# Optimization experiments

Measured on AMD Instinct MI355X. Metric: run time of the kernel, lower is better.

## Reference

```python
import jax, jax.numpy as jnp
import numpy as np

K = 3
STRIDE = 1
PAD = 1


def _conv2d(x, w, b):
    y = jax.lax.conv_general_dilated(
        x, w, window_strides=(STRIDE, STRIDE),
        padding=[(PAD, PAD), (PAD, PAD)],
        dimension_numbers=("NCHW", "OIHW", "NCHW"))
    return y + b[None, :, None, None]


def _bilinear_sample(xb, py, px):
    # xb: [C, H, W]; py, px: [K2, Ho, Wo] float sample coords
    C, H, W = xb.shape
    y0 = jnp.floor(py)
    x0 = jnp.floor(px)
    ay = py - y0  # frac weights
    ax = px - x0
    out = jnp.zeros((C,) + py.shape, dtype=xb.dtype)
    corners = [
        (y0, x0, (1.0 - ay) * (1.0 - ax)),
        (y0, x0 + 1.0, (1.0 - ay) * ax),
        (y0 + 1.0, x0, ay * (1.0 - ax)),
        (y0 + 1.0, x0 + 1.0, ay * ax),
    ]
    for yc, xc, wgt in corners:
        valid = (yc >= 0) & (yc < H) & (xc >= 0) & (xc < W)
        yi = jnp.clip(yc, 0, H - 1).astype(jnp.int32)
        xi = jnp.clip(xc, 0, W - 1).astype(jnp.int32)
        g = xb[:, yi, xi]  # [C, K2, Ho, Wo]
        out = out + g * (wgt * valid.astype(xb.dtype))[None]
    return out


def _deform_forward(x, weight, bias, p_weight, p_bias):
    B, Cin, H, W = x.shape
    Cout = weight.shape[0]
    K2 = K * K
    # offset / mask prediction conv
    pout = _conv2d(x, p_weight, p_bias)  # [B, 3*K2, Ho, Wo]
    o1, o2, m = jnp.split(pout, 3, axis=1)
    offset = jnp.concatenate([o1, o2], axis=1)  # [B, 2*K2, Ho, Wo]
    mask = jax.nn.sigmoid(m)  # [B, K2, Ho, Wo]
    Ho, Wo = mask.shape[2], mask.shape[3]
    # torchvision layout: channel 2k = dy_k, 2k+1 = dx_k
    off = offset.reshape(B, K2, 2, Ho, Wo)
    dy, dx = off[:, :, 0], off[:, :, 1]  # [B, K2, Ho, Wo]
    ki = (jnp.arange(K2) // K).astype(x.dtype)  # kernel row
    kj = (jnp.arange(K2) % K).astype(x.dtype)   # kernel col
    base_y = jnp.arange(Ho, dtype=x.dtype) * STRIDE - PAD  # [Ho]
    base_x = jnp.arange(Wo, dtype=x.dtype) * STRIDE - PAD  # [Wo]
    py = base_y[None, None, :, None] + ki[None, :, None, None] + dy
    px = base_x[None, None, None, :] + kj[None, :, None, None] + dx
    sampled = jax.vmap(_bilinear_sample)(x, py, px)  # [B, Cin, K2, Ho, Wo]
    sampled = sampled * mask[:, None]
    w = weight.reshape(Cout, Cin, K2)
    out = jnp.einsum('bckhw,ock->bohw', sampled, w) + bias[None, :, None, None]
    return out


def setup_inputs() -> dict:
    key = jax.random.key(0)
    k1, k2, k3 = jax.random.split(key, 3)
    B, Cin, Cout, H, W = 4, 256, 256, 64, 64
    x = jax.random.normal(k1, (B, Cin, H, W), dtype=jnp.float32)
    fan_in = Cin * K * K
    weight = jax.random.normal(k2, (Cout, Cin, K, K), dtype=jnp.float32) / np.sqrt(fan_in)
    bias = jnp.zeros((Cout,), dtype=jnp.float32)
    # small random offset/mask predictor (zero-init in the original; randomized
    # here so the deformable sampling path is exercised)
    p_weight = jax.random.normal(k3, (3 * K * K, Cin, K, K), dtype=jnp.float32) * 0.02
    p_bias = jnp.zeros((3 * K * K,), dtype=jnp.float32)
    return {"x": x, "weight": weight, "bias": bias, "p_weight": p_weight, "p_bias": p_bias}


def reference(x, weight, bias, p_weight, p_bias):
    return _deform_forward(x, weight, bias, p_weight, p_bias)
```

## Files before the change

kernel.cpp:

```cpp
#include <hip/hip_runtime.h>
#include <stdint.h>


#define CIN 256
#define COUT 256
#define HWS 4096
#define MTOT 16384
#define KTOT 2304
#define SPLITK 8

typedef __attribute__((ext_vector_type(8))) short bf16x8;
typedef __attribute__((ext_vector_type(4))) float f32x4;

__device__ __forceinline__ unsigned short f2bf(float f) {
  unsigned int u = __float_as_uint(f);
  unsigned int r = (u + 0x7fffu + ((u >> 16) & 1u)) >> 16;
  return (unsigned short)r;
}
__device__ __forceinline__ float bf2f(unsigned short u) {
  return __uint_as_float(((unsigned int)u) << 16);
}
__device__ __forceinline__ float bflo(unsigned int u) { return __uint_as_float(u << 16); }
__device__ __forceinline__ float bfhi(unsigned int u) { return __uint_as_float(u & 0xffff0000u); }

__device__ __forceinline__ void gload_lds16(const void* g, void* l) {
  __builtin_amdgcn_global_load_lds((const __attribute__((address_space(1))) void*)g,
                                   (__attribute__((address_space(3))) void*)l, 16, 0, 0);
}

#define GLOAD8(D, P)  asm volatile("global_load_dwordx2 %0, %1, off" : "=v"(D) : "v"(P))
#define GLOAD16(D, P) asm volatile("global_load_dwordx4 %0, %1, off" : "=v"(D) : "v"(P))
#define WAITVM(N)                                            \
  {                                                          \
    asm volatile("s_waitcnt vmcnt(" #N ")" ::: "memory");    \
    __builtin_amdgcn_sched_barrier(0);                       \
  }
#define BARRIER_LGKM                                                  \
  { asm volatile("s_waitcnt lgkmcnt(0)\n\ts_barrier" ::: "memory"); }

__global__ __launch_bounds__(256) void prep_and_transpose(const float* __restrict__ x,
                                                          const float* __restrict__ w,
                                                          const float* __restrict__ pw,
                                                          unsigned short* __restrict__ xt,
                                                          unsigned short* __restrict__ WB,
                                                          unsigned short* __restrict__ PWs,
                                                          unsigned short* __restrict__ zerop) {
  __shared__ float tile[32][33];
  int bid = blockIdx.x;
  if (bid < 4096) {
    int b = bid >> 10;
    int rest = bid & 1023;
    int hw0 = (rest & 127) * 32;
    int c0 = ((rest >> 7) & 7) * 32;
    int tx = threadIdx.x & 31, ty = threadIdx.x >> 5;
    for (int i = ty; i < 32; i += 8)
      tile[i][tx] = x[(size_t)(b * CIN + c0 + i) * HWS + hw0 + tx];
    __syncthreads();
    for (int r = ty; r < 32; r += 8)
      xt[(size_t)(b * HWS + hw0 + r) * CIN + c0 + tx] = f2bf(tile[tx][r]);
  } else {
    int idx = (bid - 4096) * 256 + threadIdx.x;
    if (idx < 512)
      *(uint4*)(zerop + idx * 8) = make_uint4(0, 0, 0, 0);
    if (idx < KTOT * COUT) {
      int f = idx;
      int e = f & 7;
      int row = (f >> 3) & 15;
      int quad = (f >> 7) & 3;
      int j = (f >> 9) & 15;
      int t = f >> 13;
      int kk = t * 32 + quad * 8 + e;
      int o = j * 16 + row;
      int k = kk >> 8, c = kk & 255;
      WB[f] = f2bf(w[o * KTOT + c * 9 + k]);
    } else {
      int f2 = idx - KTOT * COUT;
      int t_ = f2 & 7;
      int rest = f2 >> 3;
      int j = rest & 31;
      int kk = (rest >> 5) * 8 + t_;
      int k = kk >> 8, c = kk & 255;
      float v = (j < 27) ? pw[j * KTOT + c * 9 + k] : 0.0f;
      PWs[f2] = f2bf(v);
    }
  }
}

__global__ __launch_bounds__(256) void offset_conv_sk(const unsigned short* __restrict__ xt,
                                                      const unsigned short* __restrict__ PWs,
                                                      const unsigned short* __restrict__ zerop,
                                                      float* __restrict__ Pbuf) {
  __shared__ unsigned short Al[64 * 32];
  __shared__ unsigned short Bl[1024];
  int tid = threadIdx.x;
  int lane = tid & 63, wv = tid >> 6;
  int mt = (blockIdx.x & 7) * 32 + (blockIdx.x >> 3);
  int m0 = mt * 64;
  int s = blockIdx.y;
  int b = m0 >> 12;
  int hw0 = m0 & 4095;
  f32x4 acc[2] = {};

  for (int tt = 0; tt < 72 / SPLITK; ++tt) {
    int t = s * (72 / SPLITK) + tt;
    int k = t >> 3, c0 = (t & 7) * 32;
    int dyk = k / 3 - 1;
    int dxk = k % 3 - 1;
    __syncthreads();
    if (tid < 128)
      gload_lds16(PWs + (size_t)t * 1024 + tid * 8, &Bl[tid * 8]);
    {
      int r = tid >> 2;
      int hw = hw0 + r;
      int h = hw >> 6, wwp = hw & 63;
      int y = h + dyk, xx = wwp + dxk;
      bool valid = ((unsigned)y < 64u) && ((unsigned)xx < 64u);
      const unsigned short* src = valid
          ? xt + ((size_t)((b << 12) + (y << 6) + xx) << 8) + c0 + (tid & 3) * 8
          : zerop;
      gload_lds16(src, &Al[tid * 8]);
    }
    __syncthreads();
    int row = lane & 15, quad = lane >> 4;
    bf16x8 af = *(const bf16x8*)&Al[(wv * 16 + row) * 32 + quad * 8];
    for (int j = 0; j < 2; ++j) {
      bf16x8 bfr = *(const bf16x8*)&Bl[(quad * 32 + j * 16 + row) * 8];
      acc[j] = __builtin_amdgcn_mfma_f32_16x16x32_bf16(af, bfr, acc[j], 0, 0, 0);
    }
  }

  int row = lane & 15, quad = lane >> 4;
  for (int j = 0; j < 2; ++j) {
    int n = j * 16 + row;
    for (int r_ = 0; r_ < 4; ++r_) {
      int m = m0 + wv * 16 + quad * 4 + r_;
      Pbuf[((size_t)s * MTOT + m) * 32 + n] = acc[j][r_];
    }
  }
}

__global__ __launch_bounds__(256) void index_prep(const float* __restrict__ Pbuf,
                                                  const float* __restrict__ p_bias,
                                                  int4* __restrict__ DIW) {
  int gid = blockIdx.x * 256 + threadIdx.x;
  int m = gid / 9;
  int k = gid - m * 9;

  float dy = p_bias[2 * k];
  float dx = p_bias[2 * k + 1];
  float mv = p_bias[18 + k];
#pragma unroll
  for (int s = 0; s < SPLITK; ++s) {
    const float* p = Pbuf + ((size_t)s * MTOT + m) * 32;
    dy += p[2 * k];
    dx += p[2 * k + 1];
    mv += p[18 + k];
  }
  float mk = 1.0f / (1.0f + __expf(-mv));

  int hw = m & 4095, h = hw >> 6, ww = hw & 63;
  float py = (float)(h - 1 + k / 3) + dy;
  float px = (float)(ww - 1 + k % 3) + dx;
  float y0f = floorf(py), x0f = floorf(px);
  float ay = py - y0f, ax = px - x0f;
  int y0 = (int)y0f, x0 = (int)x0f;

  float w00 = (1.f - ay) * (1.f - ax) * mk;
  float w01 = (1.f - ay) * ax * mk;
  float w10 = ay * (1.f - ax) * mk;
  float w11 = ay * ax * mk;

  float vy0 = ((unsigned)y0 < 64u) ? 1.f : 0.f;
  float vy1 = ((unsigned)(y0 + 1) < 64u) ? 1.f : 0.f;
  float vx0 = ((unsigned)x0 < 64u) ? 1.f : 0.f;
  float vx1 = ((unsigned)(x0 + 1) < 64u) ? 1.f : 0.f;
  w00 *= vy0 * vx0; w01 *= vy0 * vx1; w10 *= vy1 * vx0; w11 *= vy1 * vx1;

  int yc0 = min(max(y0, 0), 63), yc1 = min(max(y0 + 1, 0), 63);
  int xc0 = min(max(x0, 0), 63), xc1 = min(max(x0 + 1, 0), 63);

  DIW[(size_t)gid * 2] = make_int4((yc0 * 64 + xc0) * 256, (yc0 * 64 + xc1) * 256,
                                   (yc1 * 64 + xc0) * 256, (yc1 * 64 + xc1) * 256);
  float4 w4 = make_float4(w00, w01, w10, w11);
  ((float4*)DIW)[(size_t)gid * 2 + 1] = w4;
}

__device__ __forceinline__ void bilin4p(const uint2 c00, const uint2 c01,
                                        const uint2 c10, const uint2 c11,
                                        const float4 w4, unsigned short* dst) {
  float v0 = w4.x * bflo(c00.x) + w4.y * bflo(c01.x) + w4.z * bflo(c10.x) + w4.w * bflo(c11.x);
  float v1 = w4.x * bfhi(c00.x) + w4.y * bfhi(c01.x) + w4.z * bfhi(c10.x) + w4.w * bfhi(c11.x);
  float v2 = w4.x * bflo(c00.y) + w4.y * bflo(c01.y) + w4.z * bflo(c10.y) + w4.w * bflo(c11.y);
  float v3 = w4.x * bfhi(c00.y) + w4.y * bfhi(c01.y) + w4.z * bfhi(c10.y) + w4.w * bfhi(c11.y);
  ushort4 o;
  o.x = f2bf(v0); o.y = f2bf(v1); o.z = f2bf(v2); o.w = f2bf(v3);
  *(ushort4*)dst = o;
}

#define MFMA8(A0, A1, A2_, A3, B0, B1)                                                   \
  acc[0][0] = __builtin_amdgcn_mfma_f32_16x16x32_bf16(A0, B0, acc[0][0], 0, 0, 0);       \
  acc[0][1] = __builtin_amdgcn_mfma_f32_16x16x32_bf16(A0, B1, acc[0][1], 0, 0, 0);       \
  acc[1][0] = __builtin_amdgcn_mfma_f32_16x16x32_bf16(A1, B0, acc[1][0], 0, 0, 0);       \
  acc[1][1] = __builtin_amdgcn_mfma_f32_16x16x32_bf16(A1, B1, acc[1][1], 0, 0, 0);       \
  acc[2][0] = __builtin_amdgcn_mfma_f32_16x16x32_bf16(A2_, B0, acc[2][0], 0, 0, 0);      \
  acc[2][1] = __builtin_amdgcn_mfma_f32_16x16x32_bf16(A2_, B1, acc[2][1], 0, 0, 0);      \
  acc[3][0] = __builtin_amdgcn_mfma_f32_16x16x32_bf16(A3, B0, acc[3][0], 0, 0, 0);       \
  acc[3][1] = __builtin_amdgcn_mfma_f32_16x16x32_bf16(A3, B1, acc[3][1], 0, 0, 0);

#define FITER_S(T, PAR, GI0, GI1, GI2, GI3, GC0, GC1, GC2, GC3, BC0, BC1, BN0, BN1)      \
  {                                                                                      \
    if ((((T) + 2) & 7) == 0) dI4 = Tbl[r][((T) + 2) >> 3][0];                           \
    int cq = (((T) + 2) & 7) * 32 + qo;                                                  \
    GLOAD8(GI0, xtb + dI4.x + cq);                                                       \
    GLOAD8(GI1, xtb + dI4.y + cq);                                                       \
    GLOAD8(GI2, xtb + dI4.z + cq);                                                       \
    GLOAD8(GI3, xtb + dI4.w + cq);                                                       \
    const unsigned short* bt_ = bpb + (size_t)((T) + 1) * 8192;                          \
    GLOAD16(BN0, bt_);                                                                   \
    GLOAD16(BN1, bt_ + 512);                                                             \
    afr0 = *(const bf16x8*)&As[PAR][row][quad * 8];                                      \
    afr1 = *(const bf16x8*)&As[PAR][16 + row][quad * 8];                                 \
    afr2 = *(const bf16x8*)&As[PAR][32 + row][quad * 8];                                 \
    afr3 = *(const bf16x8*)&As[PAR][48 + row][quad * 8];                                 \
    if ((((T) + 1) & 7) == 0) dW4 = *(float4*)&Tbl[r][((T) + 1) >> 3][1];                \
    WAITVM(8)                                                                            \
    bilin4p(GC0, GC1, GC2, GC3, dW4, &As[PAR ^ 1][r][qo]);                               \
    WAITVM(6)                                                                            \
    MFMA8(afr0, afr1, afr2, afr3, BC0, BC1)                                              \
    BARRIER_LGKM                                                                         \
  }

__global__ __launch_bounds__(512, 2) void fused_gemm(const unsigned short* __restrict__ xt,
                                                     const int4* __restrict__ DIW,
                                                     const unsigned short* __restrict__ WB,
                                                     const float* __restrict__ bias,
                                                     float* __restrict__ out) {
  __shared__ unsigned short As[2][64][40];
  __shared__ int4 Tbl[64][9][2];

  int tid = threadIdx.x;
  int lane = tid & 63, wv = tid >> 6;
  int mt = (blockIdx.x & 7) * 32 + (blockIdx.x >> 3);
  int mb = mt * 64;
  int b = mb >> 12;
  int hw0 = mb & 4095;
  const unsigned short* xtb = xt + ((size_t)b << 20);

  {
    const int4* src = DIW + (size_t)mb * 18;
    int4* dst = (int4*)Tbl;
    for (int i = tid; i < 1152; i += 512)
      gload_lds16(src + i, dst + i);
  }
  __syncthreads();

  int r = tid >> 3;
  int qo = (tid & 7) * 4;

  int4 dI4 = Tbl[r][0][0];
  float4 dW4 = *(float4*)&Tbl[r][0][1];

  int row = lane & 15, quad = lane >> 4;
  const unsigned short* bpb = WB + (size_t)(wv * 2) * 512 + quad * 128 + row * 8;

  f32x4 acc[4][2] = {};
  uint2 gA0, gA1, gA2, gA3;
  uint2 gB0, gB1, gB2, gB3;
  bf16x8 bA0, bA1, bB0, bB1;
  bf16x8 afr0, afr1, afr2, afr3;

  {
    uint2 p00 = *(const uint2*)(xtb + dI4.x + qo);
    uint2 p01 = *(const uint2*)(xtb + dI4.y + qo);
    uint2 p10 = *(const uint2*)(xtb + dI4.z + qo);
    uint2 p11 = *(const uint2*)(xtb + dI4.w + qo);
    bilin4p(p00, p01, p10, p11, dW4, &As[0][r][qo]);
    GLOAD8(gB0, xtb + dI4.x + 32 + qo);
    GLOAD8(gB1, xtb + dI4.y + 32 + qo);
    GLOAD8(gB2, xtb + dI4.z + 32 + qo);
    GLOAD8(gB3, xtb + dI4.w + 32 + qo);
    GLOAD16(bA0, bpb);
    GLOAD16(bA1, bpb + 512);
  }
  BARRIER_LGKM

#pragma unroll 1
  for (int t = 0; t < 70; t += 2) {
    FITER_S(t,     0, gA0, gA1, gA2, gA3, gB0, gB1, gB2, gB3, bA0, bA1, bB0, bB1)
    FITER_S(t + 1, 1, gB0, gB1, gB2, gB3, gA0, gA1, gA2, gA3, bB0, bB1, bA0, bA1)
  }

  {
    const unsigned short* bt_ = bpb + (size_t)71 * 8192;
    GLOAD16(bB0, bt_);
    GLOAD16(bB1, bt_ + 512);
    afr0 = *(const bf16x8*)&As[0][row][quad * 8];
    afr1 = *(const bf16x8*)&As[0][16 + row][quad * 8];
    afr2 = *(const bf16x8*)&As[0][32 + row][quad * 8];
    afr3 = *(const bf16x8*)&As[0][48 + row][quad * 8];
    WAITVM(4)
    bilin4p(gB0, gB1, gB2, gB3, dW4, &As[1][r][qo]);
    WAITVM(2)
    MFMA8(afr0, afr1, afr2, afr3, bA0, bA1)
    BARRIER_LGKM
  }
  {
    afr0 = *(const bf16x8*)&As[1][row][quad * 8];
    afr1 = *(const bf16x8*)&As[1][16 + row][quad * 8];
    afr2 = *(const bf16x8*)&As[1][32 + row][quad * 8];
    afr3 = *(const bf16x8*)&As[1][48 + row][quad * 8];
    WAITVM(0)
    MFMA8(afr0, afr1, afr2, afr3, bB0, bB1)
  }

#pragma unroll
  for (int j = 0; j < 2; ++j) {
    int o = wv * 32 + j * 16 + row;
    float bo = bias[o];
#pragma unroll
    for (int i = 0; i < 4; ++i) {
      int hw = hw0 + i * 16 + quad * 4;
      float4 v;
      v.x = acc[i][j][0] + bo;
      v.y = acc[i][j][1] + bo;
      v.z = acc[i][j][2] + bo;
      v.w = acc[i][j][3] + bo;
      *(float4*)(out + (((size_t)(b * COUT + o)) << 12) + hw) = v;
    }
  }
}

extern "C" void kernel_launch(void* const* d_in, const int* in_sizes, int n_in,
                              void* d_out, int out_size, void* d_ws, size_t ws_size,
                              hipStream_t stream) {
  const float* x        = (const float*)d_in[0];
  const float* weight   = (const float*)d_in[1];
  const float* bias     = (const float*)d_in[2];
  const float* p_weight = (const float*)d_in[3];
  const float* p_bias   = (const float*)d_in[4];
  float* out = (float*)d_out;
  char* ws = (char*)d_ws;

  const size_t OFF_XT   = 0;
  const size_t OFF_WB   = OFF_XT + 8388608;
  const size_t OFF_PW   = OFF_WB + 1179648;
  const size_t OFF_P    = OFF_PW + 147456;
  const size_t OFF_ZP   = OFF_P + 16777216;
  const size_t OFF_DIW  = OFF_ZP + 8192;

  unsigned short* xt    = (unsigned short*)(ws + OFF_XT);
  unsigned short* WB    = (unsigned short*)(ws + OFF_WB);
  unsigned short* PWs   = (unsigned short*)(ws + OFF_PW);
  float* Pbuf           = (float*)(ws + OFF_P);
  unsigned short* zerop = (unsigned short*)(ws + OFF_ZP);
  int4* DIW             = (int4*)(ws + OFF_DIW);

  prep_and_transpose<<<4096 + 2592, 256, 0, stream>>>(x, weight, p_weight, xt, WB, PWs, zerop);
  offset_conv_sk<<<dim3(MTOT / 64, SPLITK), 256, 0, stream>>>(xt, PWs, zerop, Pbuf);
  index_prep<<<576, 256, 0, stream>>>(Pbuf, p_bias, DIW);
  fused_gemm<<<256, 512, 0, stream>>>(xt, DIW, WB, bias, out);
}
```

Before: 133.7 us.

## Double K-step per pipeline stage to 64 and swizzle A tile in LDS

The fused gather+GEMM main loop now processes two 32-wide K slices per stage (64 channels), halving the number of barriers and loop iterations. Each stage issues eight gather loads and four B-fragment loads and runs sixteen MFMAs. The A tile grows from 40 to 64 shorts per row, and an XOR swizzle replaces the padding to avoid LDS bank conflicts. B loads are no longer prefetched one stage ahead; they are issued in the same stage they are consumed. This trades B-load latency hiding and extra registers for fewer synchronizations.

```diff
diff --git a/kernel.cpp b/kernel.cpp
--- a/kernel.cpp
+++ b/kernel.cpp
@@ -37,6 +37,8 @@
   }
 #define BARRIER_LGKM                                                  \
   { asm volatile("s_waitcnt lgkmcnt(0)\n\ts_barrier" ::: "memory"); }
+
+#define ASW(c, rr) ((c) ^ (((rr) & 7) << 3))
 
 __global__ __launch_bounds__(256) void prep_and_transpose(const float* __restrict__ x,
                                                           const float* __restrict__ w,
@@ -197,36 +199,56 @@
   *(ushort4*)dst = o;
 }
 
-#define MFMA8(A0, A1, A2_, A3, B0, B1)                                                   \
-  acc[0][0] = __builtin_amdgcn_mfma_f32_16x16x32_bf16(A0, B0, acc[0][0], 0, 0, 0);       \
-  acc[0][1] = __builtin_amdgcn_mfma_f32_16x16x32_bf16(A0, B1, acc[0][1], 0, 0, 0);       \
-  acc[1][0] = __builtin_amdgcn_mfma_f32_16x16x32_bf16(A1, B0, acc[1][0], 0, 0, 0);       \
-  acc[1][1] = __builtin_amdgcn_mfma_f32_16x16x32_bf16(A1, B1, acc[1][1], 0, 0, 0);       \
-  acc[2][0] = __builtin_amdgcn_mfma_f32_16x16x32_bf16(A2_, B0, acc[2][0], 0, 0, 0);      \
-  acc[2][1] = __builtin_amdgcn_mfma_f32_16x16x32_bf16(A2_, B1, acc[2][1], 0, 0, 0);      \
-  acc[3][0] = __builtin_amdgcn_mfma_f32_16x16x32_bf16(A3, B0, acc[3][0], 0, 0, 0);       \
-  acc[3][1] = __builtin_amdgcn_mfma_f32_16x16x32_bf16(A3, B1, acc[3][1], 0, 0, 0);
-
-#define FITER_S(T, PAR, GI0, GI1, GI2, GI3, GC0, GC1, GC2, GC3, BC0, BC1, BN0, BN1)      \
+#define MFMA16P                                                                          \
+  acc[0][0] = __builtin_amdgcn_mfma_f32_16x16x32_bf16(afr0, bB0, acc[0][0], 0, 0, 0);    \
+  acc[0][1] = __builtin_amdgcn_mfma_f32_16x16x32_bf16(afr0, bB1, acc[0][1], 0, 0, 0);    \
+  acc[1][0] = __builtin_amdgcn_mfma_f32_16x16x32_bf16(afr1, bB0, acc[1][0], 0, 0, 0);    \
+  acc[1][1] = __builtin_amdgcn_mfma_f32_16x16x32_bf16(afr1, bB1, acc[1][1], 0, 0, 0);    \
+  acc[2][0] = __builtin_amdgcn_mfma_f32_16x16x32_bf16(afr2, bB0, acc[2][0], 0, 0, 0);    \
+  acc[2][1] = __builtin_amdgcn_mfma_f32_16x16x32_bf16(afr2, bB1, acc[2][1], 0, 0, 0);    \
+  acc[3][0] = __builtin_amdgcn_mfma_f32_16x16x32_bf16(afr3, bB0, acc[3][0], 0, 0, 0);    \
+  acc[3][1] = __builtin_amdgcn_mfma_f32_16x16x32_bf16(afr3, bB1, acc[3][1], 0, 0, 0);    \
+  acc[0][0] = __builtin_amdgcn_mfma_f32_16x16x32_bf16(afr4, bB2, acc[0][0], 0, 0, 0);    \
+  acc[0][1] = __builtin_amdgcn_mfma_f32_16x16x32_bf16(afr4, bB3, acc[0][1], 0, 0, 0);    \
+  acc[1][0] = __builtin_amdgcn_mfma_f32_16x16x32_bf16(afr5, bB2, acc[1][0], 0, 0, 0);    \
+  acc[1][1] = __builtin_amdgcn_mfma_f32_16x16x32_bf16(afr5, bB3, acc[1][1], 0, 0, 0);    \
+  acc[2][0] = __builtin_amdgcn_mfma_f32_16x16x32_bf16(afr6, bB2, acc[2][0], 0, 0, 0);    \
+  acc[2][1] = __builtin_amdgcn_mfma_f32_16x16x32_bf16(afr6, bB3, acc[2][1], 0, 0, 0);    \
+  acc[3][0] = __builtin_amdgcn_mfma_f32_16x16x32_bf16(afr7, bB2, acc[3][0], 0, 0, 0);    \
+  acc[3][1] = __builtin_amdgcn_mfma_f32_16x16x32_bf16(afr7, bB3, acc[3][1], 0, 0, 0);
+
+#define FITER_P(P, PAR, GI0, GI1, GI2, GI3, GI4, GI5, GI6, GI7,                          \
+                GC0, GC1, GC2, GC3, GC4, GC5, GC6, GC7)                                  \
   {                                                                                      \
-    if ((((T) + 2) & 7) == 0) dI4 = Tbl[r][((T) + 2) >> 3][0];                           \
-    int cq = (((T) + 2) & 7) * 32 + qo;                                                  \
-    GLOAD8(GI0, xtb + dI4.x + cq);                                                       \
-    GLOAD8(GI1, xtb + dI4.y + cq);                                                       \
-    GLOAD8(GI2, xtb + dI4.z + cq);                                                       \
-    GLOAD8(GI3, xtb + dI4.w + cq);                                                       \
-    const unsigned short* bt_ = bpb + (size_t)((T) + 1) * 8192;                          \
-    GLOAD16(BN0, bt_);                                                                   \
-    GLOAD16(BN1, bt_ + 512);                                                             \
-    afr0 = *(const bf16x8*)&As[PAR][row][quad * 8];                                      \
-    afr1 = *(const bf16x8*)&As[PAR][16 + row][quad * 8];                                 \
-    afr2 = *(const bf16x8*)&As[PAR][32 + row][quad * 8];                                 \
-    afr3 = *(const bf16x8*)&As[PAR][48 + row][quad * 8];                                 \
-    if ((((T) + 1) & 7) == 0) dW4 = *(float4*)&Tbl[r][((T) + 1) >> 3][1];                \
+    const unsigned short* bt0 = bpb + (size_t)(2 * (P)) * 8192;                          \
+    GLOAD16(bB0, bt0);                                                                   \
+    GLOAD16(bB1, bt0 + 512);                                                             \
+    GLOAD16(bB2, bt0 + 8192);                                                            \
+    GLOAD16(bB3, bt0 + 8192 + 512);                                                      \
+    if ((((P) + 2) & 3) == 0) dI4 = Tbl[r][((P) + 2) >> 2][0];                           \
+    int cb = ((2 * (P) + 4) & 7) * 32 + qo;                                              \
+    GLOAD8(GI0, xtb + dI4.x + cb);                                                       \
+    GLOAD8(GI1, xtb + dI4.y + cb);                                                       \
+    GLOAD8(GI2, xtb + dI4.z + cb);                                                       \
+    GLOAD8(GI3, xtb + dI4.w + cb);                                                       \
+    GLOAD8(GI4, xtb + dI4.x + cb + 32);                                                  \
+    GLOAD8(GI5, xtb + dI4.y + cb + 32);                                                  \
+    GLOAD8(GI6, xtb + dI4.z + cb + 32);                                                  \
+    GLOAD8(GI7, xtb + dI4.w + cb + 32);                                                  \
+    afr0 = *(const bf16x8*)&As[PAR][row][ASW(quad * 8, row)];                            \
+    afr1 = *(const bf16x8*)&As[PAR][16 + row][ASW(quad * 8, row)];                       \
+    afr2 = *(const bf16x8*)&As[PAR][32 + row][ASW(quad * 8, row)];                       \
+    afr3 = *(const bf16x8*)&As[PAR][48 + row][ASW(quad * 8, row)];                       \
+    afr4 = *(const bf16x8*)&As[PAR][row][ASW(32 + quad * 8, row)];                       \
+    afr5 = *(const bf16x8*)&As[PAR][16 + row][ASW(32 + quad * 8, row)];                  \
+    afr6 = *(const bf16x8*)&As[PAR][32 + row][ASW(32 + quad * 8, row)];                  \
+    afr7 = *(const bf16x8*)&As[PAR][48 + row][ASW(32 + quad * 8, row)];                  \
+    if ((((P) + 1) & 3) == 0) dW4 = *(float4*)&Tbl[r][((P) + 1) >> 2][1];                \
+    WAITVM(12)                                                                           \
+    bilin4p(GC0, GC1, GC2, GC3, dW4, &As[PAR ^ 1][r][ASW(qo, r)]);                       \
+    bilin4p(GC4, GC5, GC6, GC7, dW4, &As[PAR ^ 1][r][ASW(32 + qo, r)]);                  \
     WAITVM(8)                                                                            \
-    bilin4p(GC0, GC1, GC2, GC3, dW4, &As[PAR ^ 1][r][qo]);                               \
-    WAITVM(6)                                                                            \
-    MFMA8(afr0, afr1, afr2, afr3, BC0, BC1)                                              \
+    MFMA16P                                                                              \
     BARRIER_LGKM                                                                         \
   }
 
@@ -235,7 +257,7 @@
                                                      const unsigned short* __restrict__ WB,
                                                      const float* __restrict__ bias,
                                                      float* __restrict__ out) {
-  __shared__ unsigned short As[2][64][40];
+  __shared__ unsigned short As[2][64][64];
   __shared__ int4 Tbl[64][9][2];
 
   int tid = threadIdx.x;
@@ -264,53 +286,78 @@
   const unsigned short* bpb = WB + (size_t)(wv * 2) * 512 + quad * 128 + row * 8;
 
   f32x4 acc[4][2] = {};
-  uint2 gA0, gA1, gA2, gA3;
-  uint2 gB0, gB1, gB2, gB3;
-  bf16x8 bA0, bA1, bB0, bB1;
-  bf16x8 afr0, afr1, afr2, afr3;
+  uint2 gA0, gA1, gA2, gA3, gA4, gA5, gA6, gA7;
+  uint2 gB0, gB1, gB2, gB3, gB4, gB5, gB6, gB7;
+  bf16x8 bB0, bB1, bB2, bB3;
+  bf16x8 afr0, afr1, afr2, afr3, afr4, afr5, afr6, afr7;
 
   {
     uint2 p00 = *(const uint2*)(xtb + dI4.x + qo);
     uint2 p01 = *(const uint2*)(xtb + dI4.y + qo);
     uint2 p10 = *(const uint2*)(xtb + dI4.z + qo);
     uint2 p11 = *(const uint2*)(xtb + dI4.w + qo);
-    bilin4p(p00, p01, p10, p11, dW4, &As[0][r][qo]);
-    GLOAD8(gB0, xtb + dI4.x + 32 + qo);
-    GLOAD8(gB1, xtb + dI4.y + 32 + qo);
-    GLOAD8(gB2, xtb + dI4.z + 32 + qo);
-    GLOAD8(gB3, xtb + dI4.w + 32 + qo);
-    GLOAD16(bA0, bpb);
-    GLOAD16(bA1, bpb + 512);
+    bilin4p(p00, p01, p10, p11, dW4, &As[0][r][ASW(qo, r)]);
+    p00 = *(const uint2*)(xtb + dI4.x + 32 + qo);
+    p01 = *(const uint2*)(xtb + dI4.y + 32 + qo);
+    p10 = *(const uint2*)(xtb + dI4.z + 32 + qo);
+    p11 = *(const uint2*)(xtb + dI4.w + 32 + qo);
+    bilin4p(p00, p01, p10, p11, dW4, &As[0][r][ASW(32 + qo, r)]);
+    GLOAD8(gB0, xtb + dI4.x + 64 + qo);
+    GLOAD8(gB1, xtb + dI4.y + 64 + qo);
+    GLOAD8(gB2, xtb + dI4.z + 64 + qo);
+    GLOAD8(gB3, xtb + dI4.w + 64 + qo);
+    GLOAD8(gB4, xtb + dI4.x + 96 + qo);
+    GLOAD8(gB5, xtb + dI4.y + 96 + qo);
+    GLOAD8(gB6, xtb + dI4.z + 96 + qo);
+    GLOAD8(gB7, xtb + dI4.w + 96 + qo);
   }
   BARRIER_LGKM
 
 #pragma unroll 1
-  for (int t = 0; t < 70; t += 2) {
-    FITER_S(t,     0, gA0, gA1, gA2, gA3, gB0, gB1, gB2, gB3, bA0, bA1, bB0, bB1)
-    FITER_S(t + 1, 1, gB0, gB1, gB2, gB3, gA0, gA1, gA2, gA3, bB0, bB1, bA0, bA1)
+  for (int p = 0; p < 34; p += 2) {
+    FITER_P(p,     0, gA0, gA1, gA2, gA3, gA4, gA5, gA6, gA7,
+                      gB0, gB1, gB2, gB3, gB4, gB5, gB6, gB7)
+    FITER_P(p + 1, 1, gB0, gB1, gB2, gB3, gB4, gB5, gB6, gB7,
+                      gA0, gA1, gA2, gA3, gA4, gA5, gA6, gA7)
   }
 
   {
-    const unsigned short* bt_ = bpb + (size_t)71 * 8192;
-    GLOAD16(bB0, bt_);
-    GLOAD16(bB1, bt_ + 512);
-    afr0 = *(const bf16x8*)&As[0][row][quad * 8];
-    afr1 = *(const bf16x8*)&As[0][16 + row][quad * 8];
-    afr2 = *(const bf16x8*)&As[0][32 + row][quad * 8];
-    afr3 = *(const bf16x8*)&As[0][48 + row][quad * 8];
+    const unsigned short* bt0 = bpb + (size_t)68 * 8192;
+    GLOAD16(bB0, bt0);
+    GLOAD16(bB1, bt0 + 512);
+    GLOAD16(bB2, bt0 + 8192);
+    GLOAD16(bB3, bt0 + 8192 + 512);
+    afr0 = *(const bf16x8*)&As[0][row][ASW(quad * 8, row)];
+    afr1 = *(const bf16x8*)&As[0][16 + row][ASW(quad * 8, row)];
+    afr2 = *(const bf16x8*)&As[0][32 + row][ASW(quad * 8, row)];
+    afr3 = *(const bf16x8*)&As[0][48 + row][ASW(quad * 8, row)];
+    afr4 = *(const bf16x8*)&As[0][row][ASW(32 + quad * 8, row)];
+    afr5 = *(const bf16x8*)&As[0][16 + row][ASW(32 + quad * 8, row)];
+    afr6 = *(const bf16x8*)&As[0][32 + row][ASW(32 + quad * 8, row)];
+    afr7 = *(const bf16x8*)&As[0][48 + row][ASW(32 + quad * 8, row)];
     WAITVM(4)
-    bilin4p(gB0, gB1, gB2, gB3, dW4, &As[1][r][qo]);
-    WAITVM(2)
-    MFMA8(afr0, afr1, afr2, afr3, bA0, bA1)
+    bilin4p(gB0, gB1, gB2, gB3, dW4, &As[1][r][ASW(qo, r)]);
+    bilin4p(gB4, gB5, gB6, gB7, dW4, &As[1][r][ASW(32 + qo, r)]);
+    WAITVM(0)
+    MFMA16P
     BARRIER_LGKM
   }
   {
-    afr0 = *(const bf16x8*)&As[1][row][quad * 8];
-    afr1 = *(const bf16x8*)&As[1][16 + row][quad * 8];
-    afr2 = *(const bf16x8*)&As[1][32 + row][quad * 8];
-    afr3 = *(const bf16x8*)&As[1][48 + row][quad * 8];
+    const unsigned short* bt0 = bpb + (size_t)70 * 8192;
+    GLOAD16(bB0, bt0);
+    GLOAD16(bB1, bt0 + 512);
+    GLOAD16(bB2, bt0 + 8192);
+    GLOAD16(bB3, bt0 + 8192 + 512);
+    afr0 = *(const bf16x8*)&As[1][row][ASW(quad * 8, row)];
+    afr1 = *(const bf16x8*)&As[1][16 + row][ASW(quad * 8, row)];
+    afr2 = *(const bf16x8*)&As[1][32 + row][ASW(quad * 8, row)];
+    afr3 = *(const bf16x8*)&As[1][48 + row][ASW(quad * 8, row)];
+    afr4 = *(const bf16x8*)&As[1][row][ASW(32 + quad * 8, row)];
+    afr5 = *(const bf16x8*)&As[1][16 + row][ASW(32 + quad * 8, row)];
+    afr6 = *(const bf16x8*)&As[1][32 + row][ASW(32 + quad * 8, row)];
+    afr7 = *(const bf16x8*)&As[1][48 + row][ASW(32 + quad * 8, row)];
     WAITVM(0)
-    MFMA8(afr0, afr1, afr2, afr3, bB0, bB1)
+    MFMA16P
   }
 
 #pragma unroll
```

Measured after the change: 137.1 us. 1.03x slower.
